# Optimization experiments

Measured on AMD Instinct MI355X. Metric: run time of the kernel, lower is better.

## Reference

```python
import jax, jax.numpy as jnp
import numpy as np

D_MODEL = 1024
NUM_HEADS = 16
D_K = D_MODEL // NUM_HEADS
SCALE = float(np.sqrt(D_K))


def setup_inputs() -> dict:
    key = jax.random.key(0)
    ks = jax.random.split(key, 6)
    x = jax.random.normal(ks[0], (2, 2048, D_MODEL), dtype=jnp.float32)
    s = 1.0 / np.sqrt(D_MODEL)
    w_q = jax.random.uniform(ks[1], (D_MODEL, D_MODEL), jnp.float32, -s, s)
    w_k = jax.random.uniform(ks[2], (D_MODEL, D_MODEL), jnp.float32, -s, s)
    w_v = jax.random.uniform(ks[3], (D_MODEL, D_MODEL), jnp.float32, -s, s)
    w_o = jax.random.uniform(ks[4], (D_MODEL, D_MODEL), jnp.float32, -s, s)
    b_o = jax.random.uniform(ks[5], (D_MODEL,), jnp.float32, -s, s)
    return {"x": x, "w_q": w_q, "w_k": w_k, "w_v": w_v, "w_o": w_o, "b_o": b_o}


def reference(x, w_q, w_k, w_v, w_o, b_o):
    B, S, _ = x.shape
    # project and split heads: [B, H, S, d_k]
    def heads(w):
        return (x @ w.T).reshape(B, S, NUM_HEADS, D_K).transpose(0, 2, 1, 3)
    Q, K, V = heads(w_q), heads(w_k), heads(w_v)
    scores = jnp.einsum("bhqd,bhkd->bhqk", Q, K) / SCALE  # [B,H,S,S]
    attn = jax.nn.softmax(scores, axis=-1)
    context = jnp.einsum("bhqk,bhkd->bhqd", attn, V)
    context = context.transpose(0, 2, 1, 3).reshape(B, S, D_MODEL)
    return context @ w_o.T + b_o
```

## Files before the change

### kernel.cpp

```cpp
#include <hip/hip_runtime.h>

typedef unsigned short u16t;
typedef short bf16x8 __attribute__((ext_vector_type(8)));
typedef short bf16x4 __attribute__((ext_vector_type(4)));
typedef float f32x4 __attribute__((ext_vector_type(4)));

#define NHEADS 16
#define SEQ 2048
#define DMODEL 1024
#define HEAD_ELEMS (SEQ * 64)
#define LSTR 72
#define MATE ((size_t)2 * SEQ * DMODEL)
#define CSC 0.1803368801f
#define MB 4.0f

__device__ __forceinline__ u16t f2bf(float f) {
  union { float f; unsigned u; } v; v.f = f;
  unsigned r = v.u + 0x7FFFu + ((v.u >> 16) & 1u);
  return (u16t)(r >> 16);
}
__device__ __forceinline__ float bf2f(u16t b) {
  union { unsigned u; float f; } v; v.u = ((unsigned)b) << 16;
  return v.f;
}
__device__ __forceinline__ float sanef(float x) {
  return fminf(fmaxf(x, -16384.f), 16384.f);
}
__device__ __forceinline__ unsigned pk2(float a, float b) {
  union { float f; unsigned u; } x, y; x.f = a; y.f = b;
  return __builtin_amdgcn_perm(y.u + 0x8000u, x.u + 0x8000u, 0x07060302u);
}
__device__ __forceinline__ unsigned cvtpk2(float a, float b) {
  unsigned r;
  asm("v_cvt_pk_bf16_f32 %0, %1, %2" : "=v"(r) : "v"(a), "v"(b));
  return r;
}
__device__ __forceinline__ bf16x8 cvt8(const float* p) {
  const f32x4* q4 = (const f32x4*)p;
  f32x4 a = q4[0], b = q4[1];
  bf16x8 o;
  o[0] = (short)f2bf(a[0]); o[1] = (short)f2bf(a[1]);
  o[2] = (short)f2bf(a[2]); o[3] = (short)f2bf(a[3]);
  o[4] = (short)f2bf(b[0]); o[5] = (short)f2bf(b[1]);
  o[6] = (short)f2bf(b[2]); o[7] = (short)f2bf(b[3]);
  return o;
}

__device__ __forceinline__ void stage16(const u16t* g, u16t* l) {
  __builtin_amdgcn_global_load_lds(
      (const __attribute__((address_space(1))) unsigned int*)g,
      (__attribute__((address_space(3))) unsigned int*)l, 16, 0, 0);
}

struct ushort4a { u16t x, y, z, w; } __attribute__((aligned(8)));

__device__ __forceinline__ int detect_bf16_wave(const u16t* p) {
  int lane = threadIdx.x & 63;
  int cnt = 0;
#pragma unroll
  for (int i = 0; i < 8; ++i) {
    int ex = (p[2 * (lane * 8 + i)] >> 7) & 0xFF;
    cnt += (ex >= 100 && ex <= 140) ? 1 : 0;
  }
  cnt += __shfl_xor(cnt, 1);
  cnt += __shfl_xor(cnt, 2);
  cnt += __shfl_xor(cnt, 4);
  cnt += __shfl_xor(cnt, 8);
  cnt += __shfl_xor(cnt, 16);
  cnt += __shfl_xor(cnt, 32);
  return cnt >= 300;
}

__global__ __launch_bounds__(256) void qkv_kernel(
    const void* __restrict__ xv,
    const void* __restrict__ wqv, const void* __restrict__ wkv,
    const void* __restrict__ wvv,
    u16t* __restrict__ q_ws, u16t* __restrict__ k_ws, u16t* __restrict__ vt_ws) {
  __shared__ u16t As[128 * 32];
  __shared__ u16t Bs[128 * 32];
  const int bfm = detect_bf16_wave((const u16t*)xv);
  const int tid = threadIdx.x;
  const int bm0 = blockIdx.x * 128;
  const int bn0 = blockIdx.y * 128;
  const int z = blockIdx.z;
  const void* Wv = (z == 0) ? wqv : ((z == 1) ? wkv : wvv);
  const float scale = (z == 0) ? CSC : 1.0f;
  const int lane = tid & 63;
  const int w = tid >> 6;
  const int ln = lane & 15;
  const int quad = lane >> 4;
  const int wm = (w & 1) * 64;
  const int wn = (w >> 1) * 64;

  f32x4 acc[4][4] = {};

  for (int kt = 0; kt < 32; ++kt) {
    __syncthreads();
    if (bfm) {
      const u16t* x = (const u16t*)xv;
      const u16t* W = (const u16t*)Wv;
#pragma unroll
      for (int j = 0; j < 2; ++j) {
        int f = j * 256 + tid;
        int row = f >> 2;
        int col = (f & 3) * 8;
        stage16(x + (size_t)(bm0 + row) * DMODEL + kt * 32 + col, &As[f * 8]);
        stage16(W + (size_t)(bn0 + row) * DMODEL + kt * 32 + col, &Bs[f * 8]);
      }
    } else {
      const float* x = (const float*)xv;
      const float* W = (const float*)Wv;
#pragma unroll
      for (int j = 0; j < 2; ++j) {
        int f = j * 256 + tid;
        int row = f >> 2;
        int col = (f & 3) * 8;
        *(bf16x8*)&As[f * 8] = cvt8(x + (size_t)(bm0 + row) * DMODEL + kt * 32 + col);
        *(bf16x8*)&Bs[f * 8] = cvt8(W + (size_t)(bn0 + row) * DMODEL + kt * 32 + col);
      }
    }
    __syncthreads();
    bf16x8 a[4], b[4];
#pragma unroll
    for (int t = 0; t < 4; ++t)
      a[t] = *(const bf16x8*)&As[(wm + t * 16 + ln) * 32 + quad * 8];
#pragma unroll
    for (int t = 0; t < 4; ++t)
      b[t] = *(const bf16x8*)&Bs[(wn + t * 16 + ln) * 32 + quad * 8];
#pragma unroll
    for (int i = 0; i < 4; ++i)
#pragma unroll
      for (int jn = 0; jn < 4; ++jn)
        acc[i][jn] = __builtin_amdgcn_mfma_f32_16x16x32_bf16(a[i], b[jn], acc[i][jn], 0, 0, 0);
  }

#pragma unroll
  for (int i = 0; i < 4; ++i) {
    int m_base = bm0 + wm + i * 16 + quad * 4;
#pragma unroll
    for (int jn = 0; jn < 4; ++jn) {
      int n = bn0 + wn + jn * 16 + ln;
      int h = n >> 6, dk = n & 63;
      if (z < 2) {
        u16t* dst = (z == 0) ? q_ws : k_ws;
#pragma unroll
        for (int r = 0; r < 4; ++r) {
          int m = m_base + r;
          int bb = m >> 11, s = m & 2047;
          dst[(size_t)(bb * NHEADS + h) * HEAD_ELEMS + s * 64 + dk] =
              f2bf(sanef(acc[i][jn][r]) * scale);
        }
      } else {
        int bb = m_base >> 11, s = m_base & 2047;
        ushort4a pk;
        pk.x = f2bf(sanef(acc[i][jn][0]));
        pk.y = f2bf(sanef(acc[i][jn][1]));
        pk.z = f2bf(sanef(acc[i][jn][2]));
        pk.w = f2bf(sanef(acc[i][jn][3]));
        *(ushort4a*)&vt_ws[(size_t)(bb * NHEADS + h) * HEAD_ELEMS + (size_t)dk * SEQ + s] = pk;
      }
    }
  }
}

__global__ __launch_bounds__(256, 2) void attn_kernel(
    const u16t* __restrict__ q_ws, const u16t* __restrict__ k_ws,
    const u16t* __restrict__ vt_ws, u16t* __restrict__ ctx_ws) {
  __shared__ u16t Ks[2][64 * LSTR];
  __shared__ u16t Vt[2][64 * LSTR];
  const int tid = threadIdx.x;
  const int w = tid >> 6;
  const int lane = tid & 63;
  const int ln = lane & 15;
  const int quad = lane >> 4;
  const int bh = blockIdx.y;
  const size_t base = (size_t)bh * HEAD_ELEMS;
  const int q0w = blockIdx.x * 128 + w * 32;

  bf16x8 aq[2][2];
#pragma unroll
  for (int qq = 0; qq < 2; ++qq)
#pragma unroll
    for (int ks = 0; ks < 2; ++ks)
      aq[qq][ks] = *(const bf16x8*)(q_ws + base +
          (size_t)(q0w + qq * 16 + ln) * 64 + ks * 32 + quad * 8);

  bf16x8 vone;
#pragma unroll
  for (int i = 0; i < 8; ++i) vone[i] = (short)0x3F80;

  const int r0 = tid >> 3;
  const int cc = (tid & 7) * 8;
  const u16t* kp = k_ws + base + (size_t)tid * 8;
  const u16t* vp = vt_ws + base + (size_t)r0 * SEQ + cc;
  const int d0 = r0 * LSTR + cc;
  const int d1 = (r0 + 32) * LSTR + cc;

  f32x4 accO[2][4] = {};
  f32x4 accL[2] = {};

  *(bf16x8*)&Ks[0][d0] = *(const bf16x8*)kp;
  *(bf16x8*)&Ks[0][d1] = *(const bf16x8*)(kp + 2048);
  *(bf16x8*)&Vt[0][d0] = *(const bf16x8*)vp;
  *(bf16x8*)&Vt[0][d1] = *(const bf16x8*)(vp + 32 * SEQ);
  __syncthreads();

  for (int kt = 0; kt < 32; ++kt) {
    const int cur = kt & 1;
    bf16x8 rk0, rk1, rv0, rv1;
    if (kt < 31) {
      kp += 4096;
      vp += 64;
      rk0 = *(const bf16x8*)kp;
      rk1 = *(const bf16x8*)(kp + 2048);
      rv0 = *(const bf16x8*)vp;
      rv1 = *(const bf16x8*)(vp + 32 * SEQ);
    }
    const u16t* Kc = Ks[cur];
    const u16t* Vc = Vt[cur];

    f32x4 st[2][4];
#pragma unroll
    for (int qq = 0; qq < 2; ++qq)
#pragma unroll
      for (int nt = 0; nt < 4; ++nt) {
        st[qq][nt][0] = -MB; st[qq][nt][1] = -MB;
        st[qq][nt][2] = -MB; st[qq][nt][3] = -MB;
      }
#pragma unroll
    for (int nt = 0; nt < 4; ++nt)
#pragma unroll
      for (int ks = 0; ks < 2; ++ks) {
        bf16x8 bk = *(const bf16x8*)&Kc[(nt * 16 + ln) * LSTR + ks * 32 + quad * 8];
#pragma unroll
        for (int qq = 0; qq < 2; ++qq)
          st[qq][nt] = __builtin_amdgcn_mfma_f32_16x16x32_bf16(bk, aq[qq][ks], st[qq][nt], 0, 0, 0);
      }

#pragma unroll
    for (int pp = 0; pp < 2; ++pp) {
      union { unsigned u[4]; bf16x8 v; } ap[2];
#pragma unroll
      for (int qq = 0; qq < 2; ++qq) {
        float pv[8];
#pragma unroll
        for (int j = 0; j < 4; ++j) {
          pv[j]     = exp2f(st[qq][2 * pp][j]);
          pv[4 + j] = exp2f(st[qq][2 * pp + 1][j]);
        }
        ap[qq].u[0] = cvtpk2(pv[0], pv[1]);
        ap[qq].u[1] = cvtpk2(pv[2], pv[3]);
        ap[qq].u[2] = cvtpk2(pv[4], pv[5]);
        ap[qq].u[3] = cvtpk2(pv[6], pv[7]);
        accL[qq] = __builtin_amdgcn_mfma_f32_16x16x32_bf16(ap[qq].v, vone, accL[qq], 0, 0, 0);
      }
#pragma unroll
      for (int dt = 0; dt < 4; ++dt) {
        const u16t* vrow = &Vc[(dt * 16 + ln) * LSTR + quad * 4];
        bf16x4 lo = *(const bf16x4*)(vrow + (2 * pp) * 16);
        bf16x4 hi = *(const bf16x4*)(vrow + (2 * pp + 1) * 16);
        bf16x8 bb = __builtin_shufflevector(lo, hi, 0, 1, 2, 3, 4, 5, 6, 7);
#pragma unroll
        for (int qq = 0; qq < 2; ++qq)
          accO[qq][dt] = __builtin_amdgcn_mfma_f32_16x16x32_bf16(ap[qq].v, bb, accO[qq][dt], 0, 0, 0);
      }
    }

    if (kt < 31) {
      *(bf16x8*)&Ks[cur ^ 1][d0] = rk0;
      *(bf16x8*)&Ks[cur ^ 1][d1] = rk1;
      *(bf16x8*)&Vt[cur ^ 1][d0] = rv0;
      *(bf16x8*)&Vt[cur ^ 1][d1] = rv1;
      __syncthreads();
    }
  }

#pragma unroll
  for (int qq = 0; qq < 2; ++qq) {
    float inv[4];
#pragma unroll
    for (int rr = 0; rr < 4; ++rr)
      inv[rr] = 1.0f / fmaxf(accL[qq][rr], 1e-20f);
#pragma unroll
    for (int dt = 0; dt < 4; ++dt)
#pragma unroll
      for (int rr = 0; rr < 4; ++rr)
        ctx_ws[base + (size_t)(q0w + qq * 16 + quad * 4 + rr) * 64 + dt * 16 + ln] =
            f2bf(accO[qq][dt][rr] * inv[rr]);
  }
}

__global__ __launch_bounds__(256, 4) void outproj_kernel(
    const u16t* __restrict__ ctx, const void* __restrict__ wov,
    const void* __restrict__ bov_, void* __restrict__ outv) {
  __shared__ u16t As[2][64 * LSTR];
  __shared__ u16t Bs[2][64 * LSTR];
  const int bfm = detect_bf16_wave((const u16t*)wov);
  const int tid = threadIdx.x;
  const int bm0 = blockIdx.x * 64;
  const int bn0 = blockIdx.y * 64;
  const int lane = tid & 63;
  const int w = tid >> 6;
  const int ln = lane & 15;
  const int quad = lane >> 4;
  const int wm = (w & 1) * 32;
  const int wn = (w >> 1) * 32;

  f32x4 acc[2][2] = {};

  auto do_mfma = [&](int cur) {
    bf16x8 a[2][2], b[2][2];
#pragma unroll
    for (int t = 0; t < 2; ++t)
#pragma unroll
      for (int ks = 0; ks < 2; ++ks) {
        a[t][ks] = *(const bf16x8*)&As[cur][(wm + t * 16 + ln) * LSTR + ks * 32 + quad * 8];
        b[t][ks] = *(const bf16x8*)&Bs[cur][(wn + t * 16 + ln) * LSTR + ks * 32 + quad * 8];
      }
#pragma unroll
    for (int p = 0; p < 2; ++p)
#pragma unroll
      for (int q = 0; q < 2; ++q)
#pragma unroll
        for (int ks = 0; ks < 2; ++ks)
          acc[p][q] = __builtin_amdgcn_mfma_f32_16x16x32_bf16(a[p][ks], b[q][ks], acc[p][q], 0, 0, 0);
  };

  const int c0 = tid, c1 = tid + 256;
  const int r0 = c0 >> 3, o0 = (c0 & 7) * 8;
  const int r1 = c1 >> 3, o1 = (c1 & 7) * 8;
  const int d0 = r0 * LSTR + o0, d1 = r1 * LSTR + o1;
  const int m0 = bm0 + r0, m1 = bm0 + r1;
  const u16t* ap0 = ctx + (size_t)((m0 >> 11) * NHEADS) * HEAD_ELEMS + (m0 & 2047) * 64 + o0;
  const u16t* ap1 = ctx + (size_t)((m1 >> 11) * NHEADS) * HEAD_ELEMS + (m1 & 2047) * 64 + o1;

  if (bfm) {
    const u16t* wo = (const u16t*)wov;
    const u16t* bp0 = wo + (size_t)(bn0 + r0) * DMODEL + o0;
    const u16t* bp1 = wo + (size_t)(bn0 + r1) * DMODEL + o1;
    bf16x8 ra0 = *(const bf16x8*)ap0, ra1 = *(const bf16x8*)ap1;
    bf16x8 rb0 = *(const bf16x8*)bp0, rb1 = *(const bf16x8*)bp1;
    *(bf16x8*)&As[0][d0] = ra0; *(bf16x8*)&As[0][d1] = ra1;
    *(bf16x8*)&Bs[0][d0] = rb0; *(bf16x8*)&Bs[0][d1] = rb1;
    __syncthreads();
    for (int kt = 0; kt < 16; ++kt) {
      int cur = kt & 1;
      if (kt < 15) {
        ap0 += HEAD_ELEMS; ap1 += HEAD_ELEMS;
        bp0 += 64; bp1 += 64;
        ra0 = *(const bf16x8*)ap0; ra1 = *(const bf16x8*)ap1;
        rb0 = *(const bf16x8*)bp0; rb1 = *(const bf16x8*)bp1;
      }
      do_mfma(cur);
      if (kt < 15) {
        int nxt = cur ^ 1;
        *(bf16x8*)&As[nxt][d0] = ra0; *(bf16x8*)&As[nxt][d1] = ra1;
        *(bf16x8*)&Bs[nxt][d0] = rb0; *(bf16x8*)&Bs[nxt][d1] = rb1;
        __syncthreads();
      }
    }
  } else {
    const float* wo = (const float*)wov;
    for (int kt = 0; kt < 16; ++kt) {
      __syncthreads();
      *(bf16x8*)&As[0][d0] = *(const bf16x8*)(ap0 + (size_t)kt * HEAD_ELEMS);
      *(bf16x8*)&As[0][d1] = *(const bf16x8*)(ap1 + (size_t)kt * HEAD_ELEMS);
      *(bf16x8*)&Bs[0][d0] = cvt8(wo + (size_t)(bn0 + r0) * DMODEL + kt * 64 + o0);
      *(bf16x8*)&Bs[0][d1] = cvt8(wo + (size_t)(bn0 + r1) * DMODEL + kt * 64 + o1);
      __syncthreads();
      do_mfma(0);
    }
  }

#pragma unroll
  for (int p = 0; p < 2; ++p) {
    int m_base = bm0 + wm + p * 16 + quad * 4;
#pragma unroll
    for (int q = 0; q < 2; ++q) {
      int n = bn0 + wn + q * 16 + ln;
      float bov = bfm ? bf2f(((const u16t*)bov_)[n]) : ((const float*)bov_)[n];
#pragma unroll
      for (int r = 0; r < 2 * 2; ++r) {
        int m = m_base + r;
        float v = sanef(acc[p][q][r] + bov);
        if (bfm) ((u16t*)outv)[(size_t)m * DMODEL + n] = f2bf(v);
        else     ((float*)outv)[(size_t)m * DMODEL + n] = v;
      }
    }
  }
}

extern "C" void kernel_launch(void* const* d_in, const int* in_sizes, int n_in,
                              void* d_out, int out_size, void* d_ws, size_t ws_size,
                              hipStream_t stream) {
  (void)in_sizes; (void)n_in; (void)out_size; (void)ws_size;
  const void* x  = d_in[0];
  const void* wq = d_in[1];
  const void* wk = d_in[2];
  const void* wv = d_in[3];
  const void* wo = d_in[4];
  const void* bo = d_in[5];

  u16t* q_ws  = (u16t*)d_ws;
  u16t* k_ws  = q_ws + MATE;
  u16t* vt_ws = k_ws + MATE;
  u16t* ctx_ws = q_ws;

  dim3 gA(32, 8, 3);
  qkv_kernel<<<gA, 256, 0, stream>>>(x, wq, wk, wv, q_ws, k_ws, vt_ws);

  dim3 gB(16, 32);
  attn_kernel<<<gB, 256, 0, stream>>>(q_ws, k_ws, vt_ws, ctx_ws);

  dim3 gC(64, 16);
  outproj_kernel<<<gC, 256, 0, stream>>>(ctx_ws, wo, bo, d_out);
}
```

Measured before the change: 206.5 us.

## Pre-convert fp32 inputs and weights to bf16 in scratch before GEMMs

Adds two elementwise conversion kernels that cast x, Wq/Wk/Wv into bf16 using the output buffer as scratch, and cast Wo and the bias into a freed workspace region after attention. The projection kernels then take their existing bf16 path (their runtime detection now sees bf16 data), which avoids per-tile fp32-to-bf16 conversion and halves operand bytes. The out-projection gets a flag so it still writes fp32 output. This adds extra kernel launches and a full read/write pass over the inputs, and relies on reusing the output buffer and workspace as scratch.

```diff
diff --git a/kernel.cpp b/kernel.cpp
--- a/kernel.cpp
+++ b/kernel.cpp
@@ -11,6 +11,7 @@
 #define HEAD_ELEMS (SEQ * 64)
 #define LSTR 72
 #define MATE ((size_t)2 * SEQ * DMODEL)
+#define WELEM ((size_t)DMODEL * DMODEL)
 #define CSC 0.1803368801f
 #define MB 4.0f
 
@@ -25,10 +26,6 @@
 }
 __device__ __forceinline__ float sanef(float x) {
   return fminf(fmaxf(x, -16384.f), 16384.f);
-}
-__device__ __forceinline__ unsigned pk2(float a, float b) {
-  union { float f; unsigned u; } x, y; x.f = a; y.f = b;
-  return __builtin_amdgcn_perm(y.u + 0x8000u, x.u + 0x8000u, 0x07060302u);
 }
 __device__ __forceinline__ unsigned cvtpk2(float a, float b) {
   unsigned r;
@@ -45,6 +42,16 @@
   o[6] = (short)f2bf(b[2]); o[7] = (short)f2bf(b[3]);
   return o;
 }
+__device__ __forceinline__ void cvt_chunk(const float* s, u16t* d) {
+  const f32x4* p = (const f32x4*)s;
+  f32x4 a = p[0], b = p[1];
+  union { unsigned u[4]; bf16x8 v; } o;
+  o.u[0] = cvtpk2(a[0], a[1]);
+  o.u[1] = cvtpk2(a[2], a[3]);
+  o.u[2] = cvtpk2(b[0], b[1]);
+  o.u[3] = cvtpk2(b[2], b[3]);
+  *(bf16x8*)d = o.v;
+}
 
 __device__ __forceinline__ void stage16(const u16t* g, u16t* l) {
   __builtin_amdgcn_global_load_lds(
@@ -69,6 +76,32 @@
   cnt += __shfl_xor(cnt, 16);
   cnt += __shfl_xor(cnt, 32);
   return cnt >= 300;
+}
+
+__global__ __launch_bounds__(256) void cvt_a_kernel(
+    const float* __restrict__ xs, const float* __restrict__ qs,
+    const float* __restrict__ ks_, const float* __restrict__ vs,
+    u16t* __restrict__ xd, u16t* __restrict__ qd,
+    u16t* __restrict__ kd, u16t* __restrict__ vd) {
+  int c = blockIdx.x * 256 + threadIdx.x;
+  const float* s; u16t* d;
+  if (c < 524288)      { s = xs  + (size_t)c * 8; d = xd + (size_t)c * 8; }
+  else if (c < 655360) { int t = c - 524288; s = qs  + (size_t)t * 8; d = qd + (size_t)t * 8; }
+  else if (c < 786432) { int t = c - 655360; s = ks_ + (size_t)t * 8; d = kd + (size_t)t * 8; }
+  else if (c < 917504) { int t = c - 786432; s = vs  + (size_t)t * 8; d = vd + (size_t)t * 8; }
+  else return;
+  cvt_chunk(s, d);
+}
+
+__global__ __launch_bounds__(256) void cvt_b_kernel(
+    const float* __restrict__ os, const float* __restrict__ bs,
+    u16t* __restrict__ od, u16t* __restrict__ bd) {
+  int c = blockIdx.x * 256 + threadIdx.x;
+  const float* s; u16t* d;
+  if (c < 131072)      { s = os + (size_t)c * 8; d = od + (size_t)c * 8; }
+  else if (c < 131200) { int t = c - 131072; s = bs + (size_t)t * 8; d = bd + (size_t)t * 8; }
+  else return;
+  cvt_chunk(s, d);
 }
 
 __global__ __launch_bounds__(256) void qkv_kernel(
@@ -292,10 +325,11 @@
 
 __global__ __launch_bounds__(256, 4) void outproj_kernel(
     const u16t* __restrict__ ctx, const void* __restrict__ wov,
-    const void* __restrict__ bov_, void* __restrict__ outv) {
+    const void* __restrict__ bov_, void* __restrict__ outv, int f32out) {
   __shared__ u16t As[2][64 * LSTR];
   __shared__ u16t Bs[2][64 * LSTR];
   const int bfm = detect_bf16_wave((const u16t*)wov);
+  const int of32 = f32out || !bfm;
   const int tid = threadIdx.x;
   const int bm0 = blockIdx.x * 64;
   const int bn0 = blockIdx.y * 64;
@@ -383,8 +417,8 @@
       for (int r = 0; r < 2 * 2; ++r) {
         int m = m_base + r;
         float v = sanef(acc[p][q][r] + bov);
-        if (bfm) ((u16t*)outv)[(size_t)m * DMODEL + n] = f2bf(v);
-        else     ((float*)outv)[(size_t)m * DMODEL + n] = v;
+        if (of32) ((float*)outv)[(size_t)m * DMODEL + n] = v;
+        else      ((u16t*)outv)[(size_t)m * DMODEL + n] = f2bf(v);
       }
     }
   }
@@ -393,7 +427,7 @@
 extern "C" void kernel_launch(void* const* d_in, const int* in_sizes, int n_in,
                               void* d_out, int out_size, void* d_ws, size_t ws_size,
                               hipStream_t stream) {
-  (void)in_sizes; (void)n_in; (void)out_size; (void)ws_size;
+  (void)n_in; (void)ws_size;
   const void* x  = d_in[0];
   const void* wq = d_in[1];
   const void* wk = d_in[2];
@@ -406,12 +440,36 @@
   u16t* vt_ws = k_ws + MATE;
   u16t* ctx_ws = q_ws;
 
+  const int x_bf16 = (in_sizes != nullptr) && (in_sizes[0] == (int)(MATE * 2));
+  const int out_ok = out_size >= (int)((MATE + 3 * WELEM) * 2);
+  const void* xu = x; const void* wqu = wq; const void* wku = wk;
+  const void* wvu = wv; const void* wou = wo; const void* bou = bo;
+  int cvt = (!x_bf16) && out_ok;
+  u16t* wo16 = k_ws;
+  u16t* bo16 = k_ws + WELEM;
+  if (cvt) {
+    u16t* x16  = (u16t*)d_out;
+    u16t* wq16 = x16 + MATE;
+    u16t* wk16 = wq16 + WELEM;
+    u16t* wv16 = wk16 + WELEM;
+    cvt_a_kernel<<<3584, 256, 0, stream>>>(
+        (const float*)x, (const float*)wq, (const float*)wk, (const float*)wv,
+        x16, wq16, wk16, wv16);
+    xu = x16; wqu = wq16; wku = wk16; wvu = wv16;
+  }
+
   dim3 gA(32, 8, 3);
-  qkv_kernel<<<gA, 256, 0, stream>>>(x, wq, wk, wv, q_ws, k_ws, vt_ws);
+  qkv_kernel<<<gA, 256, 0, stream>>>(xu, wqu, wku, wvu, q_ws, k_ws, vt_ws);
 
   dim3 gB(16, 32);
   attn_kernel<<<gB, 256, 0, stream>>>(q_ws, k_ws, vt_ws, ctx_ws);
 
+  if (cvt) {
+    cvt_b_kernel<<<513, 256, 0, stream>>>(
+        (const float*)wo, (const float*)bo, wo16, bo16);
+    wou = wo16; bou = bo16;
+  }
+
   dim3 gC(64, 16);
-  outproj_kernel<<<gC, 256, 0, stream>>>(ctx_ws, wo, bo, d_out);
-}
+  outproj_kernel<<<gC, 256, 0, stream>>>(ctx_ws, wou, bou, d_out, cvt ? 1 : 0);
+}
```

After: 204.8 us. No clear change (-0.8%).
